# Kernel optimization log

Hardware: AMD Instinct MI355X
Metric: run time of the kernel (lower is better)

The kernel has to match this reference:

```python
import jax, jax.numpy as jnp
import numpy as np


def setup_inputs() -> dict:
    key = jax.random.key(0)
    B, I, H = 8192, 1024, 1024
    C = I + H
    ks = jax.random.split(key, 7)
    # Xavier-uniform bound for Linear(C, H)
    bound = float(np.sqrt(6.0 / (C + H)))
    def xavier(k):
        return jax.random.uniform(k, (H, C), jnp.float32, -bound, bound)
    return {
        "x": jax.random.normal(ks[0], (B, I), jnp.float32),
        "h": jax.random.normal(ks[1], (B, H), jnp.float32),
        "c": jax.random.normal(ks[2], (B, H), jnp.float32),
        "W_i": xavier(ks[3]),
        "W_f": xavier(ks[4]),
        "W_o": xavier(ks[5]),
        "W_g": xavier(ks[6]),
        "b_i": jnp.zeros((H,), jnp.float32),
        "b_f": jnp.zeros((H,), jnp.float32),
        "b_o": jnp.zeros((H,), jnp.float32),
        "b_g": jnp.zeros((H,), jnp.float32),
    }


def reference(x, h, c, W_i, W_f, W_o, W_g, b_i, b_f, b_o, b_g):
    # combined: [B, input+hidden]
    combined = jnp.concatenate([x, h], axis=1)
    # fuse 4 gate GEMMs into one: W stacked -> [4H, C]
    W = jnp.concatenate([W_i, W_f, W_o, W_g], axis=0)
    b = jnp.concatenate([b_i, b_f, b_o, b_g], axis=0)
    gates = combined @ W.T + b  # [B, 4H]
    i_pre, f_pre, o_pre, g_pre = jnp.split(gates, 4, axis=1)
    i = jax.nn.sigmoid(i_pre)
    f = jax.nn.sigmoid(f_pre)
    o = jax.nn.sigmoid(o_pre)
    g = jnp.tanh(g_pre)
    c_t = f * c + i * g
    h_t = o * jnp.tanh(c_t)
    return (h_t, c_t)
```

## Files before the change

kernel.cpp:

```cpp
#include <hip/hip_runtime.h>
#include <hip/hip_bf16.h>
#include <stdint.h>


typedef __bf16 bf16x8 __attribute__((ext_vector_type(8)));
typedef __bf16 bf16x4 __attribute__((ext_vector_type(4)));
typedef float f32x4 __attribute__((ext_vector_type(4)));

#define B_DIM 8192
#define H_DIM 1024
#define C_DIM 2048

#define XH_ELEMS (B_DIM * H_DIM)
#define W_ELEMS  (H_DIM * C_DIM)
#define CVT_TOTAL (2 * XH_ELEMS + 4 * W_ELEMS)
#define WS_NEEDED ((size_t)CVT_TOTAL * 2)

__device__ __forceinline__ void async_cp16(void* lds_dst, const void* g_src) {
    __builtin_amdgcn_global_load_lds(
        (const __attribute__((address_space(1))) void*)g_src,
        (__attribute__((address_space(3))) void*)lds_dst,
        16, 0, 0);
}

__device__ __forceinline__ bf16x8 lds_read16(const void* p) {
    bf16x8 r;
    asm volatile("ds_read_b128 %0, %1"
                 : "=v"(r)
                 : "v"((const __attribute__((address_space(3))) void*)p));
    return r;
}

__global__ __launch_bounds__(256)
void cvt_kernel(const float* __restrict__ x, const float* __restrict__ h,
                const float* __restrict__ wi, const float* __restrict__ wf,
                const float* __restrict__ wo, const float* __restrict__ wg,
                __hip_bfloat16* __restrict__ dst)
{
    const size_t stride = (size_t)gridDim.x * 256;
    for (size_t t = (size_t)blockIdx.x * 256 + threadIdx.x;
         t < (size_t)(CVT_TOTAL / 8); t += stride) {
        const size_t base = t * 8;
        const float* src;
        size_t off;
        if (base < (size_t)XH_ELEMS)            { src = x; off = base; }
        else if (base < (size_t)2 * XH_ELEMS)   { src = h; off = base - XH_ELEMS; }
        else {
            const size_t wb = base - (size_t)2 * XH_ELEMS;
            const int g = (int)(wb >> 21);
            off = wb & (size_t)(W_ELEMS - 1);
            src = (g == 0) ? wi : (g == 1) ? wf : (g == 2) ? wo : wg;
        }
        const f32x4 v0 = *(const f32x4*)(src + off);
        const f32x4 v1 = *(const f32x4*)(src + off + 4);
        __hip_bfloat16 tmp[8];
        tmp[0] = __float2bfloat16(v0[0]); tmp[1] = __float2bfloat16(v0[1]);
        tmp[2] = __float2bfloat16(v0[2]); tmp[3] = __float2bfloat16(v0[3]);
        tmp[4] = __float2bfloat16(v1[0]); tmp[5] = __float2bfloat16(v1[1]);
        tmp[6] = __float2bfloat16(v1[2]); tmp[7] = __float2bfloat16(v1[3]);
        *(bf16x8*)(dst + base) = *(const bf16x8*)tmp;
    }
}

__global__ __launch_bounds__(512, 2)
void lstm_gemm_bf16(const __hip_bfloat16* __restrict__ xb,
                    const __hip_bfloat16* __restrict__ hb,
                    const __hip_bfloat16* __restrict__ Wb,
                    const float* __restrict__ c,
                    const float* __restrict__ pbi, const float* __restrict__ pbf,
                    const float* __restrict__ pbo, const float* __restrict__ pbg,
                    float* __restrict__ out)
{
    __shared__ __hip_bfloat16 lds[2][2][256][64];
    char* const ldsBase = (char*)&lds[0][0][0][0];

    const int tid  = threadIdx.x;
    const int lane = tid & 63;
    const int wave = tid >> 6;
    const int wr   = wave >> 2;
    const int wc   = wave & 3;
    const int quad = lane >> 4;
    const int l16  = lane & 15;

    const int bid = (int)blockIdx.x;
    const int swz = (bid & 7) * 64 + (bid >> 3);
    const int m_base = (swz >> 4) * 256;
    const int n0     = (swz & 15) * 64;

    uint32_t aOff[2][2], bOff[2][2];
#pragma unroll
    for (int a = 0; a < 2; ++a) {
        const int li  = a * 512 + tid;
        const int row = li >> 3;
        const int sch = ((li & 7) ^ (row & 7)) * 8;
#pragma unroll
        for (int hh = 0; hh < 2; ++hh) {
            aOff[hh][a] = (uint32_t)(m_base + hh * 128 + row) * H_DIM + (uint32_t)sch;
            const int g   = (hh << 1) | ((row >> 4) & 1);
            const int hco = ((row >> 5) << 4) | (row & 15);
            bOff[hh][a] = (uint32_t)g * (uint32_t)W_ELEMS
                        + (uint32_t)(n0 + hco) * (uint32_t)C_DIM + (uint32_t)sch;
        }
    }
    const uint32_t dstT = (uint32_t)tid * 16u;

#define STAGE_A(pO, hh, srcp, kel) do {                                                        \
    async_cp16(ldsBase + (pO) + (hh) * 16384u + 0u    + dstT, (srcp) + aOff[hh][0] + (kel));   \
    async_cp16(ldsBase + (pO) + (hh) * 16384u + 8192u + dstT, (srcp) + aOff[hh][1] + (kel));   \
} while (0)
#define STAGE_B(pO, hh, kel) do {                                                              \
    async_cp16(ldsBase + (pO) + 32768u + (hh) * 16384u + 0u    + dstT, Wb + bOff[hh][0] + (kel)); \
    async_cp16(ldsBase + (pO) + 32768u + (hh) * 16384u + 8192u + dstT, Wb + bOff[hh][1] + (kel)); \
} while (0)

    const uint32_t cb    = (uint32_t)((quad ^ (l16 & 7)) * 16);
    const uint32_t aBase = (uint32_t)(wr * 64 + l16) * 128u + cb;
    const uint32_t bBase = 32768u + (uint32_t)(wc * 32 + l16) * 128u + cb;

#define LDA(dstv, pO, ihh, ii, ss) \
    dstv = lds_read16(ldsBase + (pO) + ((aBase + (ihh) * 16384u + (ii) * 2048u) ^ ((uint32_t)(ss) << 6)))
#define LDB(dstv, pO, jj, ss) \
    dstv = lds_read16(ldsBase + (pO) + ((bBase + (((jj) >> 1)) * 16384u + ((jj) & 1) * 2048u) ^ ((uint32_t)(ss) << 6)))

    f32x4 acc[8][4];
#pragma unroll
    for (int i = 0; i < 8; ++i)
#pragma unroll
        for (int j = 0; j < 4; ++j)
            acc[i][j] = (f32x4){0.f, 0.f, 0.f, 0.f};

    STAGE_A(0u, 0, xb, 0u);
    STAGE_B(0u, 0, 0u);
    STAGE_B(0u, 1, 0u);
    STAGE_A(0u, 1, xb, 0u);
    STAGE_A(65536u, 0, xb, 64u);
    STAGE_B(65536u, 0, 64u);
    STAGE_B(65536u, 1, 64u);
    asm volatile("s_waitcnt vmcnt(6)" ::: "memory");
    __builtin_amdgcn_s_barrier();

    bf16x8 av[4][2], bv0[2][2], bv1[2][2];

    for (int u = 0; u < 32; ++u) {
        const uint32_t pO = (uint32_t)(u & 1) * 65536u;
        const uint32_t qO = pO ^ 65536u;
        const __hip_bfloat16* aS1 = (u + 1 < 16) ? xb : hb;
        const uint32_t ak1 = (uint32_t)((u + 1) & 15) * 64u;
        const __hip_bfloat16* aS2 = (u + 2 < 16) ? xb : hb;
        const uint32_t ak2 = (uint32_t)((u + 2) & 15) * 64u;
        const uint32_t bk2 = (uint32_t)(u + 2) * 64u;

#pragma unroll
        for (int i = 0; i < 4; ++i) { LDA(av[i][0], pO, 0, i, 0); LDA(av[i][1], pO, 0, i, 1); }
#pragma unroll
        for (int j = 0; j < 2; ++j) { LDB(bv0[j][0], pO, j, 0); LDB(bv0[j][1], pO, j, 1); }
        if (u < 31) STAGE_A(qO, 1, aS1, ak1);
        asm volatile("s_waitcnt lgkmcnt(8)");
        __builtin_amdgcn_s_barrier();
        asm volatile("s_waitcnt lgkmcnt(0)" ::: "memory");
        __builtin_amdgcn_sched_barrier(0);
        __builtin_amdgcn_s_setprio(1);
#pragma unroll
        for (int i = 0; i < 4; ++i)
#pragma unroll
            for (int j = 0; j < 2; ++j) {
                acc[i][j] = __builtin_amdgcn_mfma_f32_16x16x32_bf16(av[i][0], bv0[j][0], acc[i][j], 0, 0, 0);
                acc[i][j] = __builtin_amdgcn_mfma_f32_16x16x32_bf16(av[i][1], bv0[j][1], acc[i][j], 0, 0, 0);
            }
        __builtin_amdgcn_s_setprio(0);
        __builtin_amdgcn_s_barrier();

#pragma unroll
        for (int j = 0; j < 2; ++j) { LDB(bv1[j][0], pO, j + 2, 0); LDB(bv1[j][1], pO, j + 2, 1); }
        if (u < 30) STAGE_A(pO, 0, aS2, ak2);
        __builtin_amdgcn_s_barrier();
        asm volatile("s_waitcnt lgkmcnt(0)" ::: "memory");
        __builtin_amdgcn_sched_barrier(0);
        __builtin_amdgcn_s_setprio(1);
#pragma unroll
        for (int i = 0; i < 4; ++i)
#pragma unroll
            for (int j = 0; j < 2; ++j) {
                acc[i][j + 2] = __builtin_amdgcn_mfma_f32_16x16x32_bf16(av[i][0], bv1[j][0], acc[i][j + 2], 0, 0, 0);
                acc[i][j + 2] = __builtin_amdgcn_mfma_f32_16x16x32_bf16(av[i][1], bv1[j][1], acc[i][j + 2], 0, 0, 0);
            }
        __builtin_amdgcn_s_setprio(0);
        __builtin_amdgcn_s_barrier();

#pragma unroll
        for (int i = 0; i < 4; ++i) { LDA(av[i][0], pO, 1, i, 0); LDA(av[i][1], pO, 1, i, 1); }
        if (u < 30) STAGE_B(pO, 0, bk2);
        __builtin_amdgcn_s_barrier();
        asm volatile("s_waitcnt lgkmcnt(0)" ::: "memory");
        __builtin_amdgcn_sched_barrier(0);
        __builtin_amdgcn_s_setprio(1);
#pragma unroll
        for (int i = 0; i < 4; ++i)
#pragma unroll
            for (int j = 0; j < 2; ++j) {
                acc[i + 4][j] = __builtin_amdgcn_mfma_f32_16x16x32_bf16(av[i][0], bv0[j][0], acc[i + 4][j], 0, 0, 0);
                acc[i + 4][j] = __builtin_amdgcn_mfma_f32_16x16x32_bf16(av[i][1], bv0[j][1], acc[i + 4][j], 0, 0, 0);
            }
        __builtin_amdgcn_s_setprio(0);
        __builtin_amdgcn_s_barrier();

        if (u < 30) STAGE_B(pO, 1, bk2);
        __builtin_amdgcn_s_barrier();
        __builtin_amdgcn_s_setprio(1);
#pragma unroll
        for (int i = 0; i < 4; ++i)
#pragma unroll
            for (int j = 0; j < 2; ++j) {
                acc[i + 4][j + 2] = __builtin_amdgcn_mfma_f32_16x16x32_bf16(av[i][0], bv1[j][0], acc[i + 4][j + 2], 0, 0, 0);
                acc[i + 4][j + 2] = __builtin_amdgcn_mfma_f32_16x16x32_bf16(av[i][1], bv1[j][1], acc[i + 4][j + 2], 0, 0, 0);
            }
        __builtin_amdgcn_s_setprio(0);
        if (u < 30)       { asm volatile("s_waitcnt vmcnt(6)" ::: "memory"); }
        else if (u == 30) { asm volatile("s_waitcnt vmcnt(0)" ::: "memory"); }
        __builtin_amdgcn_s_barrier();
    }

#undef STAGE_A
#undef STAGE_B
#undef LDA
#undef LDB

    const int col = n0 + wc * 16 + l16;
    const float vbi = pbi[col];
    const float vbf = pbf[col];
    const float vbo = pbo[col];
    const float vbg = pbg[col];
    const size_t HB = (size_t)B_DIM * H_DIM;
#pragma unroll
    for (int i = 0; i < 8; ++i) {
        const int fb  = (i < 4) ? (wr * 64 + i * 16) : (128 + wr * 64 + (i - 4) * 16);
        const int mb0 = m_base + fb + quad * 4;
#pragma unroll
        for (int r = 0; r < 4; ++r) {
            const size_t m = (size_t)(mb0 + r);
            const float ip = acc[i][0][r] + vbi;
            const float fp = acc[i][1][r] + vbf;
            const float op = acc[i][2][r] + vbo;
            const float gp = acc[i][3][r] + vbg;
            const float ig = 1.f / (1.f + __expf(-ip));
            const float fg = 1.f / (1.f + __expf(-fp));
            const float og = 1.f / (1.f + __expf(-op));
            const float eg = __expf(-2.f * fabsf(gp));
            const float gg = copysignf((1.f - eg) / (1.f + eg), gp);
            const float cin = c[m * H_DIM + col];
            const float ct = fg * cin + ig * gg;
            const float ec = __expf(-2.f * fabsf(ct));
            const float tc = copysignf((1.f - ec) / (1.f + ec), ct);
            out[m * H_DIM + col]      = og * tc;
            out[HB + m * H_DIM + col] = ct;
        }
    }
}

#define BM 128
#define BNC 32
#define BK 64
#define K_ITERS (C_DIM / BK)

__global__ __launch_bounds__(256, 2)
void lstm_gemm_fused(const float* __restrict__ x, const float* __restrict__ h,
                     const float* __restrict__ Wi, const float* __restrict__ Wf,
                     const float* __restrict__ Wo, const float* __restrict__ Wg,
                     const float* __restrict__ c,
                     const float* __restrict__ pbi, const float* __restrict__ pbf,
                     const float* __restrict__ pbo, const float* __restrict__ pbg,
                     float* __restrict__ out)
{
    __shared__ __hip_bfloat16 As[BM][BK];
    __shared__ __hip_bfloat16 Bs[BM][BK];

    const int tid  = threadIdx.x;
    const int lane = tid & 63;
    const int wave = tid >> 6;
    const int wr   = wave >> 1;
    const int wc   = wave & 1;
    const int quad = lane >> 4;
    const int l16  = lane & 15;

    const int m_base = blockIdx.y * BM;
    const int n0     = blockIdx.x * BNC;

    const int srow = tid >> 1;
    const int scol = (tid & 1) * 32;
    const float* aS[2] = {
        x + (size_t)(m_base + srow) * H_DIM + scol,
        h + (size_t)(m_base + srow) * H_DIM + scol
    };
    const int gate = (srow >> 4) & 3;
    const int grow = n0 + ((srow >> 6) << 4) + (srow & 15);
    const float* Wsel = (gate == 0) ? Wi : (gate == 1) ? Wf : (gate == 2) ? Wo : Wg;
    const float* bS = Wsel + (size_t)grow * C_DIM + scol;

    int aRow[4], bRow[4];
#pragma unroll
    for (int i = 0; i < 4; ++i) aRow[i] = wr * 64 + i * 16 + l16;
#pragma unroll
    for (int j = 0; j < 4; ++j) bRow[j] = wc * 64 + j * 16 + l16;

    f32x4 acc[4][4];
#pragma unroll
    for (int i = 0; i < 4; ++i)
#pragma unroll
        for (int j = 0; j < 4; ++j)
            acc[i][j] = (f32x4){0.f, 0.f, 0.f, 0.f};

    for (int kt = 0; kt < K_ITERS; ++kt) {
        const int hsel = (kt >= (H_DIM / BK));
        const int koff = (kt & ((H_DIM / BK) - 1)) * BK;
        const float* ap = aS[hsel] + koff;
        const float* bp = bS + kt * BK;
        __hip_bfloat16 ta[32], tb[32];
#pragma unroll
        for (int q = 0; q < 8; ++q) {
            f32x4 a = *(const f32x4*)(ap + q * 4);
            f32x4 b = *(const f32x4*)(bp + q * 4);
            ta[q*4+0]=__float2bfloat16(a[0]); ta[q*4+1]=__float2bfloat16(a[1]);
            ta[q*4+2]=__float2bfloat16(a[2]); ta[q*4+3]=__float2bfloat16(a[3]);
            tb[q*4+0]=__float2bfloat16(b[0]); tb[q*4+1]=__float2bfloat16(b[1]);
            tb[q*4+2]=__float2bfloat16(b[2]); tb[q*4+3]=__float2bfloat16(b[3]);
        }
#pragma unroll
        for (int q = 0; q < 4; ++q) {
            const int ch  = (scol / 8) + q;
            const int sl  = ch ^ (srow & 7);
            *(bf16x8*)((char*)&As[0][0] + srow * (BK * 2) + sl * 16) = *(const bf16x8*)&ta[q * 8];
            *(bf16x8*)((char*)&Bs[0][0] + srow * (BK * 2) + sl * 16) = *(const bf16x8*)&tb[q * 8];
        }
        __syncthreads();

#pragma unroll
        for (int s = 0; s < 2; ++s) {
            bf16x8 av[4], bv[4];
#pragma unroll
            for (int i = 0; i < 4; ++i) {
                const int r  = aRow[i];
                const int ch = (s * 4 + quad) ^ (r & 7);
                av[i] = *(const bf16x8*)((const char*)&As[0][0] + r * (BK * 2) + ch * 16);
            }
#pragma unroll
            for (int j = 0; j < 4; ++j) {
                const int r  = bRow[j];
                const int ch = (s * 4 + quad) ^ (r & 7);
                bv[j] = *(const bf16x8*)((const char*)&Bs[0][0] + r * (BK * 2) + ch * 16);
            }
#pragma unroll
            for (int i = 0; i < 4; ++i)
#pragma unroll
                for (int j = 0; j < 4; ++j)
                    acc[i][j] = __builtin_amdgcn_mfma_f32_16x16x32_bf16(
                        av[i], bv[j], acc[i][j], 0, 0, 0);
        }
        __syncthreads();
    }

    const int col = n0 + wc * 16 + l16;
    const float vbi = pbi[col];
    const float vbf = pbf[col];
    const float vbo = pbo[col];
    const float vbg = pbg[col];
    const size_t HB = (size_t)B_DIM * H_DIM;
#pragma unroll
    for (int i = 0; i < 4; ++i) {
        const int mb = m_base + wr * 64 + i * 16 + quad * 4;
#pragma unroll
        for (int r = 0; r < 4; ++r) {
            const size_t m = (size_t)(mb + r);
            const float ip = acc[i][0][r] + vbi;
            const float fp = acc[i][1][r] + vbf;
            const float op = acc[i][2][r] + vbo;
            const float gp = acc[i][3][r] + vbg;
            const float ig = 1.f / (1.f + __expf(-ip));
            const float fg = 1.f / (1.f + __expf(-fp));
            const float og = 1.f / (1.f + __expf(-op));
            const float eg = __expf(-2.f * fabsf(gp));
            const float gg = copysignf((1.f - eg) / (1.f + eg), gp);
            const float cin = c[m * H_DIM + col];
            const float ct = fg * cin + ig * gg;
            const float ec = __expf(-2.f * fabsf(ct));
            const float tc = copysignf((1.f - ec) / (1.f + ec), ct);
            out[m * H_DIM + col]      = og * tc;
            out[HB + m * H_DIM + col] = ct;
        }
    }
}

extern "C" void kernel_launch(void* const* d_in, const int* in_sizes, int n_in,
                              void* d_out, int out_size, void* d_ws, size_t ws_size,
                              hipStream_t stream) {
    const float* x  = (const float*)d_in[0];
    const float* h  = (const float*)d_in[1];
    const float* c  = (const float*)d_in[2];
    const float* Wi = (const float*)d_in[3];
    const float* Wf = (const float*)d_in[4];
    const float* Wo = (const float*)d_in[5];
    const float* Wg = (const float*)d_in[6];
    const float* bi = (const float*)d_in[7];
    const float* bfp= (const float*)d_in[8];
    const float* bo = (const float*)d_in[9];
    const float* bg = (const float*)d_in[10];
    float* out = (float*)d_out;

    if (ws_size >= WS_NEEDED) {
        __hip_bfloat16* wsb = (__hip_bfloat16*)d_ws;
        cvt_kernel<<<2048, 256, 0, stream>>>(x, h, Wi, Wf, Wo, Wg, wsb);
        lstm_gemm_bf16<<<512, 512, 0, stream>>>(
            wsb, wsb + XH_ELEMS, wsb + 2 * (size_t)XH_ELEMS,
            c, bi, bfp, bo, bg, out);
    } else {
        lstm_gemm_fused<<<dim3(H_DIM / BNC, B_DIM / BM), dim3(256), 0, stream>>>(
            x, h, Wi, Wf, Wo, Wg, c, bi, bfp, bo, bg, out);
    }
}
```

Measured before the change: 306.1 us.

## Software-pipeline LDS fragment loads across MFMA quadrants with double-buffered registers

Restructures the bf16 GEMM main loop so that LDS-to-register fragment loads for the next quadrant, including the next k-tile's A and B fragments, are issued before the current quadrant's MFMAs. It double-buffers the A fragments (av0/av1) and uses partial lgkmcnt waits instead of full drains. The last iteration is peeled into an epilogue, and the MFMA order is changed to run all k-half-0 ops before k-half-1 ops. The aim is to hide LDS read latency behind matrix work. The cost is more VGPRs, and the hand-tuned waitcnt counts and the vmcnt change from 6 to 2 carry correctness risk.

```diff
diff --git a/kernel.cpp b/kernel.cpp
--- a/kernel.cpp
+++ b/kernel.cpp
@@ -4,7 +4,6 @@
 
 
 typedef __bf16 bf16x8 __attribute__((ext_vector_type(8)));
-typedef __bf16 bf16x4 __attribute__((ext_vector_type(4)));
 typedef float f32x4 __attribute__((ext_vector_type(4)));
 
 #define B_DIM 8192
@@ -139,9 +138,28 @@
     asm volatile("s_waitcnt vmcnt(6)" ::: "memory");
     __builtin_amdgcn_s_barrier();
 
-    bf16x8 av[4][2], bv0[2][2], bv1[2][2];
-
-    for (int u = 0; u < 32; ++u) {
+    bf16x8 av0[4][2], av1[4][2], bv0[2][2], bv1[2][2];
+#pragma unroll
+    for (int i = 0; i < 4; ++i) { LDA(av0[i][0], 0u, 0, i, 0); LDA(av0[i][1], 0u, 0, i, 1); }
+    LDB(bv0[0][0], 0u, 0, 0); LDB(bv0[1][0], 0u, 1, 0);
+    LDB(bv0[0][1], 0u, 0, 1); LDB(bv0[1][1], 0u, 1, 1);
+
+#define MFMA_Q(AV, BV, IOFF, JOFF) do {                                                   \
+    _Pragma("unroll")                                                                     \
+    for (int i = 0; i < 4; ++i)                                                           \
+        _Pragma("unroll")                                                                 \
+        for (int j = 0; j < 2; ++j)                                                       \
+            acc[i + (IOFF)][j + (JOFF)] = __builtin_amdgcn_mfma_f32_16x16x32_bf16(        \
+                AV[i][0], BV[j][0], acc[i + (IOFF)][j + (JOFF)], 0, 0, 0);                \
+    _Pragma("unroll")                                                                     \
+    for (int i = 0; i < 4; ++i)                                                           \
+        _Pragma("unroll")                                                                 \
+        for (int j = 0; j < 2; ++j)                                                       \
+            acc[i + (IOFF)][j + (JOFF)] = __builtin_amdgcn_mfma_f32_16x16x32_bf16(        \
+                AV[i][1], BV[j][1], acc[i + (IOFF)][j + (JOFF)], 0, 0, 0);                \
+} while (0)
+
+    for (int u = 0; u < 31; ++u) {
         const uint32_t pO = (uint32_t)(u & 1) * 65536u;
         const uint32_t qO = pO ^ 65536u;
         const __hip_bfloat16* aS1 = (u + 1 < 16) ? xb : hb;
@@ -150,76 +168,76 @@
         const uint32_t ak2 = (uint32_t)((u + 2) & 15) * 64u;
         const uint32_t bk2 = (uint32_t)(u + 2) * 64u;
 
-#pragma unroll
-        for (int i = 0; i < 4; ++i) { LDA(av[i][0], pO, 0, i, 0); LDA(av[i][1], pO, 0, i, 1); }
-#pragma unroll
-        for (int j = 0; j < 2; ++j) { LDB(bv0[j][0], pO, j, 0); LDB(bv0[j][1], pO, j, 1); }
-        if (u < 31) STAGE_A(qO, 1, aS1, ak1);
-        asm volatile("s_waitcnt lgkmcnt(8)");
+        LDB(bv1[0][0], pO, 2, 0); LDB(bv1[1][0], pO, 3, 0);
+        LDB(bv1[0][1], pO, 2, 1); LDB(bv1[1][1], pO, 3, 1);
+        STAGE_A(qO, 1, aS1, ak1);
+        __builtin_amdgcn_s_barrier();
+        asm volatile("s_waitcnt lgkmcnt(4)" ::: "memory");
+        __builtin_amdgcn_sched_barrier(0);
+        __builtin_amdgcn_s_setprio(1);
+        MFMA_Q(av0, bv0, 0, 0);
+        __builtin_amdgcn_s_setprio(0);
+        __builtin_amdgcn_s_barrier();
+
+#pragma unroll
+        for (int i = 0; i < 4; ++i) { LDA(av1[i][0], pO, 1, i, 0); LDA(av1[i][1], pO, 1, i, 1); }
+        if (u < 30) STAGE_A(pO, 0, aS2, ak2);
+        __builtin_amdgcn_s_barrier();
+        asm volatile("s_waitcnt lgkmcnt(8)" ::: "memory");
+        __builtin_amdgcn_sched_barrier(0);
+        __builtin_amdgcn_s_setprio(1);
+        MFMA_Q(av0, bv1, 0, 2);
+        __builtin_amdgcn_s_setprio(0);
+        if (u < 30)  { asm volatile("s_waitcnt vmcnt(2)" ::: "memory"); }
+        else         { asm volatile("s_waitcnt vmcnt(0)" ::: "memory"); }
+        __builtin_amdgcn_s_barrier();
+
+#pragma unroll
+        for (int i = 0; i < 4; ++i) { LDA(av0[i][0], qO, 0, i, 0); LDA(av0[i][1], qO, 0, i, 1); }
+        if (u < 30) STAGE_B(pO, 0, bk2);
+        __builtin_amdgcn_s_barrier();
+        asm volatile("s_waitcnt lgkmcnt(8)" ::: "memory");
+        __builtin_amdgcn_sched_barrier(0);
+        __builtin_amdgcn_s_setprio(1);
+        MFMA_Q(av1, bv0, 4, 0);
+        __builtin_amdgcn_s_setprio(0);
+        __builtin_amdgcn_s_barrier();
+
+        LDB(bv0[0][0], qO, 0, 0); LDB(bv0[1][0], qO, 1, 0);
+        LDB(bv0[0][1], qO, 0, 1); LDB(bv0[1][1], qO, 1, 1);
+        if (u < 30) STAGE_B(pO, 1, bk2);
+        __builtin_amdgcn_s_barrier();
+        asm volatile("s_waitcnt lgkmcnt(12)" ::: "memory");
+        __builtin_amdgcn_sched_barrier(0);
+        __builtin_amdgcn_s_setprio(1);
+        MFMA_Q(av1, bv1, 4, 2);
+        __builtin_amdgcn_s_setprio(0);
+        __builtin_amdgcn_s_barrier();
+    }
+
+    {
+        const uint32_t pO = 65536u;
+        LDB(bv1[0][0], pO, 2, 0); LDB(bv1[1][0], pO, 3, 0);
+        LDB(bv1[0][1], pO, 2, 1); LDB(bv1[1][1], pO, 3, 1);
+        __builtin_amdgcn_s_barrier();
+        asm volatile("s_waitcnt lgkmcnt(4)" ::: "memory");
+        __builtin_amdgcn_sched_barrier(0);
+        MFMA_Q(av0, bv0, 0, 0);
+        __builtin_amdgcn_s_barrier();
+#pragma unroll
+        for (int i = 0; i < 4; ++i) { LDA(av1[i][0], pO, 1, i, 0); LDA(av1[i][1], pO, 1, i, 1); }
+        __builtin_amdgcn_s_barrier();
+        asm volatile("s_waitcnt lgkmcnt(8)" ::: "memory");
+        __builtin_amdgcn_sched_barrier(0);
+        MFMA_Q(av0, bv1, 0, 2);
         __builtin_amdgcn_s_barrier();
         asm volatile("s_waitcnt lgkmcnt(0)" ::: "memory");
         __builtin_amdgcn_sched_barrier(0);
-        __builtin_amdgcn_s_setprio(1);
-#pragma unroll
-        for (int i = 0; i < 4; ++i)
-#pragma unroll
-            for (int j = 0; j < 2; ++j) {
-                acc[i][j] = __builtin_amdgcn_mfma_f32_16x16x32_bf16(av[i][0], bv0[j][0], acc[i][j], 0, 0, 0);
-                acc[i][j] = __builtin_amdgcn_mfma_f32_16x16x32_bf16(av[i][1], bv0[j][1], acc[i][j], 0, 0, 0);
-            }
-        __builtin_amdgcn_s_setprio(0);
-        __builtin_amdgcn_s_barrier();
-
-#pragma unroll
-        for (int j = 0; j < 2; ++j) { LDB(bv1[j][0], pO, j + 2, 0); LDB(bv1[j][1], pO, j + 2, 1); }
-        if (u < 30) STAGE_A(pO, 0, aS2, ak2);
-        __builtin_amdgcn_s_barrier();
-        asm volatile("s_waitcnt lgkmcnt(0)" ::: "memory");
-        __builtin_amdgcn_sched_barrier(0);
-        __builtin_amdgcn_s_setprio(1);
-#pragma unroll
-        for (int i = 0; i < 4; ++i)
-#pragma unroll
-            for (int j = 0; j < 2; ++j) {
-                acc[i][j + 2] = __builtin_amdgcn_mfma_f32_16x16x32_bf16(av[i][0], bv1[j][0], acc[i][j + 2], 0, 0, 0);
-                acc[i][j + 2] = __builtin_amdgcn_mfma_f32_16x16x32_bf16(av[i][1], bv1[j][1], acc[i][j + 2], 0, 0, 0);
-            }
-        __builtin_amdgcn_s_setprio(0);
-        __builtin_amdgcn_s_barrier();
-
-#pragma unroll
-        for (int i = 0; i < 4; ++i) { LDA(av[i][0], pO, 1, i, 0); LDA(av[i][1], pO, 1, i, 1); }
-        if (u < 30) STAGE_B(pO, 0, bk2);
-        __builtin_amdgcn_s_barrier();
-        asm volatile("s_waitcnt lgkmcnt(0)" ::: "memory");
-        __builtin_amdgcn_sched_barrier(0);
-        __builtin_amdgcn_s_setprio(1);
-#pragma unroll
-        for (int i = 0; i < 4; ++i)
-#pragma unroll
-            for (int j = 0; j < 2; ++j) {
-                acc[i + 4][j] = __builtin_amdgcn_mfma_f32_16x16x32_bf16(av[i][0], bv0[j][0], acc[i + 4][j], 0, 0, 0);
-                acc[i + 4][j] = __builtin_amdgcn_mfma_f32_16x16x32_bf16(av[i][1], bv0[j][1], acc[i + 4][j], 0, 0, 0);
-            }
-        __builtin_amdgcn_s_setprio(0);
-        __builtin_amdgcn_s_barrier();
-
-        if (u < 30) STAGE_B(pO, 1, bk2);
-        __builtin_amdgcn_s_barrier();
-        __builtin_amdgcn_s_setprio(1);
-#pragma unroll
-        for (int i = 0; i < 4; ++i)
-#pragma unroll
-            for (int j = 0; j < 2; ++j) {
-                acc[i + 4][j + 2] = __builtin_amdgcn_mfma_f32_16x16x32_bf16(av[i][0], bv1[j][0], acc[i + 4][j + 2], 0, 0, 0);
-                acc[i + 4][j + 2] = __builtin_amdgcn_mfma_f32_16x16x32_bf16(av[i][1], bv1[j][1], acc[i + 4][j + 2], 0, 0, 0);
-            }
-        __builtin_amdgcn_s_setprio(0);
-        if (u < 30)       { asm volatile("s_waitcnt vmcnt(6)" ::: "memory"); }
-        else if (u == 30) { asm volatile("s_waitcnt vmcnt(0)" ::: "memory"); }
-        __builtin_amdgcn_s_barrier();
-    }
-
+        MFMA_Q(av1, bv0, 4, 0);
+        MFMA_Q(av1, bv1, 4, 2);
+    }
+
+#undef MFMA_Q
 #undef STAGE_A
 #undef STAGE_B
 #undef LDA
```

After: 307.5 us. About the same (+0.5%).
